# Kernel tuning notes

Hardware: AMD Instinct MI355X
Metric: run time of the kernel (lower is better)

Reference implementation:

```python
import jax, jax.numpy as jnp
import numpy as np


def setup_inputs() -> dict:
    key = jax.random.key(0)
    k1, k2, k3, k4, k5 = jax.random.split(key, 5)
    B, S, H, L = 32, 4096, 512, 2
    scale = 1.0 / np.sqrt(H)
    return {
        "out": jax.random.normal(k1, (B, S, H), dtype=jnp.float32),
        "hidden": jax.random.normal(k2, (L, B, H), dtype=jnp.float32),
        "W": jax.random.normal(k3, (H, H), dtype=jnp.float32) * scale,
        "b": jax.random.normal(k4, (H,), dtype=jnp.float32) * scale,
        "v": jax.random.normal(k5, (H,), dtype=jnp.float32) * scale,
    }


def reference(out, hidden, W, b, v):
    # hidden_last: (B, 1, H) from last layer
    h_last = hidden[-1][:, None, :]
    # energy = tanh(out @ W^T + b + h_last)  -> (B, S, H)
    energy = jnp.tanh(jnp.einsum("bsh,oh->bso", out, W) + b + h_last)
    # scores = energy @ v  -> (B, S)
    scores = jnp.einsum("bsh,h->bs", energy, v)
    attn = jax.nn.softmax(scores, axis=-1)
    # context = sum_s attn[b,s] * out[b,s,:]  -> (B, H)
    context = jnp.einsum("bs,bsh->bh", attn, out)
    return (context, attn)
```

## Files before the change

### kernel.cpp

```cpp
#include <hip/hip_runtime.h>
#include <hip/hip_bf16.h>

#define B_ 32
#define S_ 4096
#define H_ 512
#define M_ (B_ * S_)
#define L_ 2

typedef __bf16 bf16;
typedef bf16 bf16x8 __attribute__((ext_vector_type(8)));
typedef float floatx2 __attribute__((ext_vector_type(2)));
typedef float floatx4 __attribute__((ext_vector_type(4)));
typedef float floatx16 __attribute__((ext_vector_type(16)));

__device__ inline bf16 f2b(float f) { return (bf16)f; }

__device__ inline float fast_tanh(float x) {
    float xc = fminf(15.0f, fmaxf(-15.0f, x));
    float e = __expf(2.0f * xc);
    return (e - 1.0f) * __builtin_amdgcn_rcpf(e + 1.0f);
}

__global__ __launch_bounds__(256) void convert_Wfrag(const float* __restrict__ W,
                                                     bf16* __restrict__ Wf) {
    int gid  = blockIdx.x * 256 + threadIdx.x;
    int lane = gid & 63;
    int ks   = (gid >> 6) & 31;
    int nt   = gid >> 11;
    int row  = nt * 32 + (lane & 31);
    int col  = ks * 16 + (lane >> 5) * 8;
    const float* src = W + (size_t)row * H_ + col;
    floatx4 f0 = *(const floatx4*)src;
    floatx4 f1 = *(const floatx4*)(src + 4);
    bf16x8 p = { f2b(f0[0]), f2b(f0[1]), f2b(f0[2]), f2b(f0[3]),
                 f2b(f1[0]), f2b(f1[1]), f2b(f1[2]), f2b(f1[3]) };
    *(bf16x8*)(Wf + (size_t)gid * 8) = p;
}

#define MT 64

__global__ __launch_bounds__(1024, 4) void scores_kernel(
    const float* __restrict__ outT,
    const bf16*  __restrict__ Wf,
    const float* __restrict__ bias,
    const float* __restrict__ hidden,
    const float* __restrict__ v,
    float* __restrict__ scores,
    float* __restrict__ pc,
    float* __restrict__ lmaxg,
    float* __restrict__ lsumg)
{
    __shared__ bf16 Alds[MT * 512];
    __shared__ float bv[2 * H_];

    const int tid  = threadIdx.x;
    const int wave = tid >> 6;
    const int lane = tid & 63;
    const int l31  = lane & 31;
    const int half = lane >> 5;

    const int m0    = blockIdx.x * MT;
    const int batch = m0 >> 12;
    const int koff  = (wave * 2) & 31;

    const bf16* wf = Wf + (size_t)wave * 16384 + lane * 8;

    bf16x8 bb[8];
    #pragma unroll
    for (int p = 0; p < 8; ++p)
        bb[p] = *(const bf16x8*)(wf + ((p + koff) & 31) * 512);

    if (tid < H_) {
        float bh = bias[tid] + hidden[(size_t)((L_ - 1) * B_ + batch) * H_ + tid];
        bv[tid * 2]     = bh;
        bv[tid * 2 + 1] = v[tid];
    }

    {
        const floatx4* src = (const floatx4*)(outT + (size_t)m0 * H_);
        #pragma unroll
        for (int it = 0; it < 4; ++it) {
            int idx = it * 1024 + tid;
            int r   = idx >> 6;
            int j   = idx & 63;
            floatx4 f0 = __builtin_nontemporal_load(src + idx * 2);
            floatx4 f1 = __builtin_nontemporal_load(src + idx * 2 + 1);
            bf16x8 p = { f2b(f0[0]), f2b(f0[1]), f2b(f0[2]), f2b(f0[3]),
                         f2b(f1[0]), f2b(f1[1]), f2b(f1[2]), f2b(f1[3]) };
            int frag = (r >> 5) * 32 + (j >> 1);
            int slot = (j & 1) * 32 + ((r + (j >> 1)) & 31);
            *(bf16x8*)&Alds[frag * 512 + slot * 8] = p;
        }
    }
    __syncthreads();

    floatx16 acc[2];
    acc[0] = (floatx16)(0.0f);
    acc[1] = (floatx16)(0.0f);

    bf16x8 aa[4][2];
    #pragma unroll
    for (int p = 0; p < 2; ++p) {
        const int kk = (p + koff) & 31;
        const int rot = (l31 + kk) & 31;
        #pragma unroll
        for (int mt = 0; mt < 2; ++mt)
            aa[p][mt] = *(const bf16x8*)
                &Alds[(mt * 32 + kk) * 512 + (half * 32 + rot) * 8];
    }

    #pragma unroll
    for (int ks = 0; ks < 32; ++ks) {
        const int bcur = ks & 7;
        const int acur = ks & 3;
        if (ks < 30) {
            const int kk = (ks + 2 + koff) & 31;
            const int rot = (l31 + kk) & 31;
            #pragma unroll
            for (int mt = 0; mt < 2; ++mt)
                aa[(ks + 2) & 3][mt] = *(const bf16x8*)
                    &Alds[(mt * 32 + kk) * 512 + (half * 32 + rot) * 8];
        }
        acc[0] = __builtin_amdgcn_mfma_f32_32x32x16_bf16(bb[bcur], aa[acur][0], acc[0], 0, 0, 0);
        acc[1] = __builtin_amdgcn_mfma_f32_32x32x16_bf16(bb[bcur], aa[acur][1], acc[1], 0, 0, 0);
        if (ks < 24)
            bb[bcur] = *(const bf16x8*)(wf + ((ks + 8 + koff) & 31) * 512);
    }

    float p0 = 0.0f, p1 = 0.0f;
    #pragma unroll
    for (int rg = 0; rg < 16; ++rg) {
        const int nl = (rg & 3) + 8 * (rg >> 2) + 4 * half;
        floatx2 bvv = *(const floatx2*)&bv[(wave * 32 + nl) * 2];
        p0 += fast_tanh(acc[0][rg] + bvv.x) * bvv.y;
        p1 += fast_tanh(acc[1][rg] + bvv.x) * bvv.y;
    }
    p0 += __shfl_xor(p0, 32);
    p1 += __shfl_xor(p1, 32);

    __syncthreads();
    float*   sred  = (float*)Alds;
    float*   pbuf  = sred + 1024;
    floatx4* pvred = (floatx4*)(pbuf + 64);

    if (lane < 32) {
        sred[wave * 64 + l31]      = p0;
        sred[wave * 64 + 32 + l31] = p1;
    }
    __syncthreads();

    if (tid < 64) {
        float sc = 0.0f;
        #pragma unroll
        for (int w = 0; w < 16; ++w) sc += sred[w * 64 + tid];
        scores[m0 + tid] = sc;
        float mx = sc;
        #pragma unroll
        for (int off = 32; off >= 1; off >>= 1) mx = fmaxf(mx, __shfl_xor(mx, off));
        float p = __expf(sc - mx);
        pbuf[tid] = p;
        float sm = p;
        #pragma unroll
        for (int off = 32; off >= 1; off >>= 1) sm += __shfl_xor(sm, off);
        if (tid == 0) { lmaxg[blockIdx.x] = mx; lsumg[blockIdx.x] = sm; }
    }
    __syncthreads();

    {
        const int c4 = tid & 127;
        const int sg = tid >> 7;
        const floatx4* op = (const floatx4*)(outT + (size_t)(m0 + sg * 8) * H_) + c4;
        floatx4 a = (floatx4)(0.0f);
        #pragma unroll
        for (int j = 0; j < 8; ++j)
            a += pbuf[sg * 8 + j] * __builtin_nontemporal_load(op + (size_t)j * 128);
        pvred[sg * 128 + c4] = a;
    }
    __syncthreads();
    if (tid < 128) {
        floatx4 r = (floatx4)(0.0f);
        #pragma unroll
        for (int sg = 0; sg < 8; ++sg) r += pvred[sg * 128 + tid];
        *(floatx4*)&pc[(size_t)blockIdx.x * H_ + tid * 4] = r;
    }
}

__global__ __launch_bounds__(256) void softmax_kernel(const float* __restrict__ scores,
                                                      float* __restrict__ attn) {
    __shared__ float red[4];
    int b = blockIdx.x, tid = threadIdx.x;
    const float* row = scores + (size_t)b * S_;
    float vals[16];
    float mx = -3.4e38f;
    #pragma unroll
    for (int i = 0; i < 16; ++i) { vals[i] = row[i * 256 + tid]; mx = fmaxf(mx, vals[i]); }
    #pragma unroll
    for (int off = 32; off >= 1; off >>= 1) mx = fmaxf(mx, __shfl_xor(mx, off));
    if ((tid & 63) == 0) red[tid >> 6] = mx;
    __syncthreads();
    mx = fmaxf(fmaxf(red[0], red[1]), fmaxf(red[2], red[3]));
    __syncthreads();
    float sum = 0.f;
    #pragma unroll
    for (int i = 0; i < 16; ++i) { vals[i] = __expf(vals[i] - mx); sum += vals[i]; }
    #pragma unroll
    for (int off = 32; off >= 1; off >>= 1) sum += __shfl_xor(sum, off);
    if ((tid & 63) == 0) red[tid >> 6] = sum;
    __syncthreads();
    float inv = 1.0f / (red[0] + red[1] + red[2] + red[3]);
    #pragma unroll
    for (int i = 0; i < 16; ++i) attn[(size_t)b * S_ + i * 256 + tid] = vals[i] * inv;
}

__global__ __launch_bounds__(256) void context_final(const float* __restrict__ pc,
                                                     const float* __restrict__ lmaxg,
                                                     const float* __restrict__ lsumg,
                                                     float* __restrict__ ctx) {
    __shared__ float e_sh[64];
    __shared__ float inv_sh;
    int b = blockIdx.x, tid = threadIdx.x;
    if (tid < 64) {
        float lm = lmaxg[b * 64 + tid];
        float mx = lm;
        #pragma unroll
        for (int off = 32; off >= 1; off >>= 1) mx = fmaxf(mx, __shfl_xor(mx, off));
        float e = __expf(lm - mx);
        e_sh[tid] = e;
        float gs = e * lsumg[b * 64 + tid];
        #pragma unroll
        for (int off = 32; off >= 1; off >>= 1) gs += __shfl_xor(gs, off);
        if (tid == 0) inv_sh = 1.0f / gs;
    }
    __syncthreads();
    float inv = inv_sh;
    const floatx2* pp = (const floatx2*)(pc + (size_t)b * 64 * H_) + tid;
    floatx2 a = (floatx2)(0.0f);
    #pragma unroll 8
    for (int j = 0; j < 64; ++j) {
        floatx2 q = __builtin_nontemporal_load(pp + (size_t)j * 256);
        a += e_sh[j] * q;
    }
    floatx2 r = a * inv;
    *(floatx2*)&ctx[(size_t)b * H_ + tid * 2] = r;
}

extern "C" void kernel_launch(void* const* d_in, const int* in_sizes, int n_in,
                              void* d_out, int out_size, void* d_ws, size_t ws_size,
                              hipStream_t stream) {
    const float* outT   = (const float*)d_in[0];
    const float* hidden = (const float*)d_in[1];
    const float* W      = (const float*)d_in[2];
    const float* bias   = (const float*)d_in[3];
    const float* v      = (const float*)d_in[4];

    float* ctx    = (float*)d_out;
    float* attn   = (float*)d_out + B_ * H_;

    const int NBLK = M_ / MT;
    float* scores = (float*)d_ws;
    bf16*  Wf     = (bf16*)((char*)d_ws + (size_t)M_ * 4);
    float* pc     = (float*)((char*)d_ws + (size_t)M_ * 4 + (size_t)H_ * H_ * 2);
    float* lmaxg  = pc + (size_t)NBLK * H_;
    float* lsumg  = lmaxg + NBLK;

    convert_Wfrag<<<128, 256, 0, stream>>>(W, Wf);
    scores_kernel<<<NBLK, 1024, 0, stream>>>(outT, Wf, bias, hidden, v,
                                             scores, pc, lmaxg, lsumg);
    softmax_kernel<<<B_, 256, 0, stream>>>(scores, attn);
    context_final<<<B_, 256, 0, stream>>>(pc, lmaxg, lsumg, ctx);
}
```

Baseline: 470.5 us.

## Split scores MFMA into two passes to cut registers and raise occupancy

Launch bounds go from a minimum of 4 to 8 waves per SIMD. To fit, the 64-row tile is now processed as two sequential 32-row passes with a single accumulator, a smaller W prefetch ring (4 instead of 8) and a 2-deep A prefetch. This lowers per-thread VGPR pressure so more waves can hide memory latency. The cost is that W fragments are reloaded from global/L2 in each pass, and the shorter prefetch depth may expose more load latency.

```diff
diff --git a/kernel.cpp b/kernel.cpp
--- a/kernel.cpp
+++ b/kernel.cpp
@@ -39,7 +39,7 @@
 
 #define MT 64
 
-__global__ __launch_bounds__(1024, 4) void scores_kernel(
+__global__ __launch_bounds__(1024, 8) void scores_kernel(
     const float* __restrict__ outT,
     const bf16*  __restrict__ Wf,
     const float* __restrict__ bias,
@@ -65,11 +65,6 @@
 
     const bf16* wf = Wf + (size_t)wave * 16384 + lane * 8;
 
-    bf16x8 bb[8];
-    #pragma unroll
-    for (int p = 0; p < 8; ++p)
-        bb[p] = *(const bf16x8*)(wf + ((p + koff) & 31) * 512);
-
     if (tid < H_) {
         float bh = bias[tid] + hidden[(size_t)((L_ - 1) * B_ + batch) * H_ + tid];
         bv[tid * 2]     = bh;
@@ -94,49 +89,48 @@
     }
     __syncthreads();
 
-    floatx16 acc[2];
-    acc[0] = (floatx16)(0.0f);
-    acc[1] = (floatx16)(0.0f);
-
-    bf16x8 aa[4][2];
-    #pragma unroll
-    for (int p = 0; p < 2; ++p) {
-        const int kk = (p + koff) & 31;
-        const int rot = (l31 + kk) & 31;
-        #pragma unroll
-        for (int mt = 0; mt < 2; ++mt)
-            aa[p][mt] = *(const bf16x8*)
-                &Alds[(mt * 32 + kk) * 512 + (half * 32 + rot) * 8];
-    }
-
-    #pragma unroll
-    for (int ks = 0; ks < 32; ++ks) {
-        const int bcur = ks & 7;
-        const int acur = ks & 3;
-        if (ks < 30) {
-            const int kk = (ks + 2 + koff) & 31;
-            const int rot = (l31 + kk) & 31;
-            #pragma unroll
-            for (int mt = 0; mt < 2; ++mt)
-                aa[(ks + 2) & 3][mt] = *(const bf16x8*)
-                    &Alds[(mt * 32 + kk) * 512 + (half * 32 + rot) * 8];
-        }
-        acc[0] = __builtin_amdgcn_mfma_f32_32x32x16_bf16(bb[bcur], aa[acur][0], acc[0], 0, 0, 0);
-        acc[1] = __builtin_amdgcn_mfma_f32_32x32x16_bf16(bb[bcur], aa[acur][1], acc[1], 0, 0, 0);
-        if (ks < 24)
-            bb[bcur] = *(const bf16x8*)(wf + ((ks + 8 + koff) & 31) * 512);
-    }
-
-    float p0 = 0.0f, p1 = 0.0f;
-    #pragma unroll
-    for (int rg = 0; rg < 16; ++rg) {
-        const int nl = (rg & 3) + 8 * (rg >> 2) + 4 * half;
-        floatx2 bvv = *(const floatx2*)&bv[(wave * 32 + nl) * 2];
-        p0 += fast_tanh(acc[0][rg] + bvv.x) * bvv.y;
-        p1 += fast_tanh(acc[1][rg] + bvv.x) * bvv.y;
-    }
-    p0 += __shfl_xor(p0, 32);
-    p1 += __shfl_xor(p1, 32);
+    float p01[2];
+    #pragma unroll
+    for (int pass = 0; pass < 2; ++pass) {
+        floatx16 acc = (floatx16)(0.0f);
+
+        bf16x8 bb[4];
+        #pragma unroll
+        for (int p = 0; p < 4; ++p)
+            bb[p] = *(const bf16x8*)(wf + ((p + koff) & 31) * 512);
+
+        bf16x8 aa[2];
+        {
+            const int rot = (l31 + koff) & 31;
+            aa[0] = *(const bf16x8*)
+                &Alds[(pass * 32 + koff) * 512 + (half * 32 + rot) * 8];
+        }
+
+        #pragma unroll
+        for (int ks = 0; ks < 32; ++ks) {
+            const int bcur = ks & 3;
+            const int ap   = ks & 1;
+            if (ks < 31) {
+                const int kk = (ks + 1 + koff) & 31;
+                const int rot = (l31 + kk) & 31;
+                aa[ap ^ 1] = *(const bf16x8*)
+                    &Alds[(pass * 32 + kk) * 512 + (half * 32 + rot) * 8];
+            }
+            acc = __builtin_amdgcn_mfma_f32_32x32x16_bf16(bb[bcur], aa[ap], acc, 0, 0, 0);
+            if (ks < 28)
+                bb[bcur] = *(const bf16x8*)(wf + ((ks + 4 + koff) & 31) * 512);
+        }
+
+        float p = 0.0f;
+        #pragma unroll
+        for (int rg = 0; rg < 16; ++rg) {
+            const int nl = (rg & 3) + 8 * (rg >> 2) + 4 * half;
+            floatx2 bvv = *(const floatx2*)&bv[(wave * 32 + nl) * 2];
+            p += fast_tanh(acc[rg] + bvv.x) * bvv.y;
+        }
+        p += __shfl_xor(p, 32);
+        p01[pass] = p;
+    }
 
     __syncthreads();
     float*   sred  = (float*)Alds;
@@ -144,8 +138,8 @@
     floatx4* pvred = (floatx4*)(pbuf + 64);
 
     if (lane < 32) {
-        sred[wave * 64 + l31]      = p0;
-        sred[wave * 64 + 32 + l31] = p1;
+        sred[wave * 64 + l31]      = p01[0];
+        sred[wave * 64 + 32 + l31] = p01[1];
     }
     __syncthreads();
 
```

Result: slower. 480.6 us (+2.1%).
